# Kernel tuning notes

Hardware: AMD Instinct MI355X
Metric: run time of the kernel (lower is better)

Reference implementation:

```python
import jax, jax.numpy as jnp
import numpy as np

NQ = 4          # n_qubits -> 2**4 = 16 amplitudes
NL = 3          # n_layers
TWO_PI = 2.0 * np.pi
BN_EPS = 1e-5


def _ry_batched(t):
    # t: [B] -> [B,2,2] complex64
    c, s = jnp.cos(t / 2), jnp.sin(t / 2)
    g = jnp.stack([jnp.stack([c, -s], -1), jnp.stack([s, c], -1)], -2)
    return g.astype(jnp.complex64)


def _ry(t):
    c, s = jnp.cos(t / 2), jnp.sin(t / 2)
    return jnp.stack([jnp.stack([c, -s]), jnp.stack([s, c])]).astype(jnp.complex64)


def _rz(t):
    e = jnp.stack([jnp.exp(-0.5j * t), jnp.exp(0.5j * t)]).astype(jnp.complex64)
    return jnp.diag(e)


def _apply_1q(state, gate, wire, batched):
    # state: [B,2,2,2,2]; gate: [2,2] or [B,2,2]
    s = jnp.moveaxis(state, wire + 1, -1)
    if batched:
        s = jnp.einsum('bij,b...j->b...i', gate, s)
    else:
        s = jnp.einsum('ij,...j->...i', gate, s)
    return jnp.moveaxis(s, -1, wire + 1)


def _apply_cnot(state, c, t):
    s = jnp.moveaxis(state, (c + 1, t + 1), (-2, -1))
    s = jnp.stack([s[..., 0, :], s[..., 1, ::-1]], axis=-2)  # flip target when control=1
    return jnp.moveaxis(s, (-2, -1), (c + 1, t + 1))


def _circuit(angles, weights):
    # angles: [B, NQ] float32; weights: [NL, NQ, 2]
    B = angles.shape[0]
    state = jnp.zeros((B,) + (2,) * NQ, jnp.complex64)
    state = state.at[(slice(None),) + (0,) * NQ].set(1.0)
    # input encoding RYs (per-sample angles -> batched gates)
    for i in range(NQ):
        state = _apply_1q(state, _ry_batched(angles[:, i]), i, True)
    for layer in range(NL):
        for i in range(NQ):
            state = _apply_1q(state, _ry(weights[layer, i, 0]), i, False)
            state = _apply_1q(state, _rz(weights[layer, i, 1]), i, False)
        for i in range(NQ - 1):
            state = _apply_cnot(state, i, i + 1)
        state = _apply_cnot(state, NQ - 1, 0)
    probs = jnp.abs(state) ** 2  # [B,2,2,2,2] real
    zs = []
    for i in range(NQ):
        axes = tuple(a for a in range(1, NQ + 1) if a != i + 1)
        pm = probs.sum(axis=axes)  # [B,2]
        zs.append(pm[:, 0] - pm[:, 1])
    return jnp.stack(zs, -1).astype(jnp.float32)  # [B,NQ]


def setup_inputs() -> dict:
    key = jax.random.key(0)
    ks = jax.random.split(key, 4)
    B = 524288
    x = jax.random.normal(ks[0], (B, 16), jnp.float32)
    weights = jax.random.normal(ks[1], (NL, NQ, 2), jnp.float32)
    fc_w = jax.random.normal(ks[2], (4, NQ), jnp.float32) / np.sqrt(NQ)
    fc_b = jax.random.normal(ks[3], (4,), jnp.float32) * 0.01
    gamma = jnp.ones((4,), jnp.float32)
    beta = jnp.zeros((4,), jnp.float32)
    return {"x": x, "weights": weights, "fc_w": fc_w, "fc_b": fc_b,
            "gamma": gamma, "beta": beta}


def reference(x, weights, fc_w, fc_b, gamma, beta):
    inp = x.reshape(x.shape[0], -1)[:, :NQ]
    mn, mx = inp.min(), inp.max()  # global min/max as in the torch code
    angles = TWO_PI * (inp - mn) / (mx - mn + 1e-8)
    q = _circuit(angles, weights)                # [B,4] PauliZ expvals
    out = q @ fc_w.T + fc_b                      # Linear(4,4)
    mean = out.mean(0)
    var = out.var(0)                             # biased, as torch BN training
    return gamma * (out - mean) / jnp.sqrt(var + BN_EPS) + beta
```

## Files before the change

kernel.cpp:

```cpp
#include <hip/hip_runtime.h>
#include <math.h>

#define TWO_PI_F 6.28318530717958647692f
#define BN_EPS_F 1e-5f
#define NB1 2048
#define NB2 1024
#define NT 256

#define BMIN_OFF 256
#define BMAX_OFF 2304
#define TAB_OFF 4352
#define SSLOT_OFF 4992

__global__ __launch_bounds__(NT) void k1_scan_tab(const float* __restrict__ x,
                                                  const float* __restrict__ w,
                                                  const float* __restrict__ fc_w,
                                                  float* __restrict__ wsf, int B) {
  int r = blockIdx.x * NT + threadIdx.x;
  float fmn = __builtin_inff(), fmx = -__builtin_inff();
  if (r < B) {
    float4 v = *(const float4*)(x + (size_t)r * 16);
    fmn = fminf(fminf(v.x, v.y), fminf(v.z, v.w));
    fmx = fmaxf(fmaxf(v.x, v.y), fmaxf(v.z, v.w));
  }
#pragma unroll
  for (int d = 32; d; d >>= 1) {
    fmn = fminf(fmn, __shfl_down(fmn, d));
    fmx = fmaxf(fmx, __shfl_down(fmx, d));
  }
  __shared__ float smn[4], smx[4];
  int wv = threadIdx.x >> 6, ln = threadIdx.x & 63;
  if (ln == 0) { smn[wv] = fmn; smx[wv] = fmx; }
  __syncthreads();
  if (threadIdx.x == 0) {
    wsf[BMIN_OFF + blockIdx.x] =
        fminf(fminf(smn[0], smn[1]), fminf(smn[2], smn[3]));
    wsf[BMAX_OFF + blockIdx.x] =
        fmaxf(fmaxf(smx[0], smx[1]), fmaxf(smx[2], smx[3]));
  }

  if (blockIdx.x == 0) {
    int tid = threadIdx.x;
    if (tid < 16) {
      float sr[16], si[16];
#pragma unroll
      for (int k = 0; k < 16; ++k) { sr[k] = (k == tid) ? 1.f : 0.f; si[k] = 0.f; }
#pragma unroll
      for (int l = 0; l < 3; ++l) {
#pragma unroll
        for (int i = 0; i < 4; ++i) {
          const int m = 8 >> i;
          float ryc, rys, rzc, rzs;
          __sincosf(0.5f * w[(l * 4 + i) * 2 + 0], &rys, &ryc);
          __sincosf(0.5f * w[(l * 4 + i) * 2 + 1], &rzs, &rzc);
#pragma unroll
          for (int k = 0; k < 16; ++k) {
            if (!(k & m)) {
              int k1 = k | m;
              float a0r = sr[k], a0i = si[k], a1r = sr[k1], a1i = si[k1];
              sr[k] = ryc * a0r - rys * a1r;
              si[k] = ryc * a0i - rys * a1i;
              sr[k1] = rys * a0r + ryc * a1r;
              si[k1] = rys * a0i + ryc * a1i;
            }
          }
#pragma unroll
          for (int k = 0; k < 16; ++k) {
            float ps = (k & m) ? rzs : -rzs;
            float rr = sr[k], ii = si[k];
            sr[k] = rr * rzc - ii * ps;
            si[k] = rr * ps + ii * rzc;
          }
        }
#pragma unroll
        for (int c = 0; c < 4; ++c) {
          const int mc = 8 >> c;
          const int mt = 8 >> ((c + 1) & 3);
#pragma unroll
          for (int k = 0; k < 16; ++k) {
            if ((k & mc) && !(k & mt)) {
              int k2 = k | mt;
              float tt;
              tt = sr[k]; sr[k] = sr[k2]; sr[k2] = tt;
              tt = si[k]; si[k] = si[k2]; si[k2] = tt;
            }
          }
        }
      }
#pragma unroll
      for (int k = 0; k < 16; ++k) {
        wsf[TAB_OFF + tid * 16 + k] = sr[k];
        wsf[TAB_OFF + 256 + tid * 16 + k] = si[k];
      }
    } else if (tid == 16) {
      for (int k = 0; k < 16; ++k)
        for (int j = 0; j < 4; ++j) {
          float s = 0.f;
          for (int i = 0; i < 4; ++i)
            s += fc_w[j * 4 + i] * ((k & (8 >> i)) ? -1.f : 1.f);
          wsf[TAB_OFF + 512 + k * 4 + j] = s;
        }
    }
  }
}

__device__ __forceinline__ void qfc_pair(const float* __restrict__ tab,
                                         const float* c0, const float* s0,
                                         const float* c1, const float* s1,
                                         float* o0, float* o1) {
  const float* __restrict__ Ur = tab;
  const float* __restrict__ Ui = tab + 256;
  const float* __restrict__ At = tab + 512;
  float A01_0[4] = {c0[0] * c0[1], c0[0] * s0[1], s0[0] * c0[1], s0[0] * s0[1]};
  float A23_0[4] = {c0[2] * c0[3], c0[2] * s0[3], s0[2] * c0[3], s0[2] * s0[3]};
  float A01_1[4] = {c1[0] * c1[1], c1[0] * s1[1], s1[0] * c1[1], s1[0] * s1[1]};
  float A23_1[4] = {c1[2] * c1[3], c1[2] * s1[3], s1[2] * c1[3], s1[2] * s1[3]};
  float yr0[16], yi0[16], yr1[16], yi1[16];
#pragma unroll
  for (int k = 0; k < 16; ++k) { yr0[k] = yi0[k] = yr1[k] = yi1[k] = 0.f; }
#pragma unroll
  for (int a = 0; a < 16; ++a) {
    float va0 = A01_0[a >> 2] * A23_0[a & 3];
    float va1 = A01_1[a >> 2] * A23_1[a & 3];
#pragma unroll
    for (int k = 0; k < 16; ++k) {
      float ur = Ur[a * 16 + k], ui = Ui[a * 16 + k];
      yr0[k] = fmaf(ur, va0, yr0[k]);
      yi0[k] = fmaf(ui, va0, yi0[k]);
      yr1[k] = fmaf(ur, va1, yr1[k]);
      yi1[k] = fmaf(ui, va1, yi1[k]);
    }
  }
#pragma unroll
  for (int j = 0; j < 4; ++j) { o0[j] = 0.f; o1[j] = 0.f; }
#pragma unroll
  for (int k = 0; k < 16; ++k) {
    float p0 = fmaf(yr0[k], yr0[k], yi0[k] * yi0[k]);
    float p1 = fmaf(yr1[k], yr1[k], yi1[k] * yi1[k]);
#pragma unroll
    for (int j = 0; j < 4; ++j) {
      float av = At[k * 4 + j];
      o0[j] = fmaf(av, p0, o0[j]);
      o1[j] = fmaf(av, p1, o1[j]);
    }
  }
}

__global__ __launch_bounds__(NT) void k2_main(const float* __restrict__ x,
                                              const float* __restrict__ wsf,
                                              float* __restrict__ sslot,
                                              float* __restrict__ out, int B) {
  const int tid = threadIdx.x;
  const int gtid = blockIdx.x * NT + tid;
  const int H = NB2 * NT;
  const int wv = tid >> 6, ln = tid & 63;
  const float* __restrict__ tab = wsf + TAB_OFF;

  float gm = __builtin_inff(), gM = -__builtin_inff();
#pragma unroll
  for (int q = 0; q < NB1 / 64; ++q) {
    int i = ln + q * 64;
    gm = fminf(gm, wsf[BMIN_OFF + i]);
    gM = fmaxf(gM, wsf[BMAX_OFF + i]);
  }
#pragma unroll
  for (int d = 32; d; d >>= 1) {
    gm = fminf(gm, __shfl_down(gm, d));
    gM = fmaxf(gM, __shfl_down(gM, d));
  }
  gm = __shfl(gm, 0);
  gM = __shfl(gM, 0);
  const float ssc = TWO_PI_F * 0.5f / (gM - gm + 1e-8f);

  const int s0 = gtid, s1 = gtid + H;
  const bool h0 = s0 < B, h1 = s1 < B;
  float4 xa = h0 ? *(const float4*)(x + (size_t)s0 * 16) : make_float4(0, 0, 0, 0);
  float4 xb = h1 ? *(const float4*)(x + (size_t)s1 * 16) : make_float4(0, 0, 0, 0);

  float a0[4] = {xa.x, xa.y, xa.z, xa.w};
  float a1[4] = {xb.x, xb.y, xb.z, xb.w};
  float c0[4], sn0[4], c1[4], sn1[4];
#pragma unroll
  for (int i = 0; i < 4; ++i) {
    __sincosf((a0[i] - gm) * ssc, &sn0[i], &c0[i]);
    __sincosf((a1[i] - gm) * ssc, &sn1[i], &c1[i]);
  }
  float o0[4], o1[4];
  qfc_pair(tab, c0, sn0, c1, sn1, o0, o1);

  if (h0)
    *(float4*)(out + (size_t)s0 * 4) = make_float4(o0[0], o0[1], o0[2], o0[3]);
  if (h1)
    *(float4*)(out + (size_t)s1 * 4) = make_float4(o1[0], o1[1], o1[2], o1[3]);

  float vals[8];
#pragma unroll
  for (int j = 0; j < 4; ++j) {
    float v0 = h0 ? o0[j] : 0.f, v1 = h1 ? o1[j] : 0.f;
    vals[j] = v0 + v1;
    vals[4 + j] = fmaf(v0, v0, v1 * v1);
  }
#pragma unroll
  for (int j = 0; j < 8; ++j) {
#pragma unroll
    for (int d = 32; d; d >>= 1) vals[j] += __shfl_down(vals[j], d);
  }
  __shared__ float red[4][8];
  if (ln == 0) {
#pragma unroll
    for (int j = 0; j < 8; ++j) red[wv][j] = vals[j];
  }
  __syncthreads();
  if (tid < 8) {
    sslot[blockIdx.x * 8 + tid] =
        red[0][tid] + red[1][tid] + red[2][tid] + red[3][tid];
  }
}

__global__ __launch_bounds__(NT) void k3_final(float* __restrict__ out,
                                               const float* __restrict__ sslot,
                                               const float* __restrict__ gamma,
                                               const float* __restrict__ beta,
                                               int B) {
  const int tid = threadIdx.x;
  const int gtid = blockIdx.x * NT + tid;
  const int H = NB2 * NT;
  const int ln = tid & 63;

  float v = 0.f;
#pragma unroll
  for (int k = 0; k < (NB2 * 8) / 64; ++k) v += sslot[k * 64 + ln];
#pragma unroll
  for (int d = 32; d >= 8; d >>= 1) v += __shfl_down(v, d);
  float st[8];
#pragma unroll
  for (int j = 0; j < 8; ++j) st[j] = __shfl(v, j);

  const float inv = 1.0f / (float)B;
  float sc[4], sh[4];
#pragma unroll
  for (int j = 0; j < 4; ++j) {
    float mean = st[j] * inv;
    float var = st[4 + j] * inv - mean * mean;
    float is = rsqrtf(var + BN_EPS_F);
    sc[j] = gamma[j] * is;
    sh[j] = beta[j] - mean * sc[j];
  }
#pragma unroll
  for (int p = 0; p < 2; ++p) {
    int s = gtid + p * H;
    if (s < B) {
      float4 q = *(float4*)(out + (size_t)s * 4);
      *(float4*)(out + (size_t)s * 4) =
          make_float4(fmaf(q.x, sc[0], sh[0]), fmaf(q.y, sc[1], sh[1]),
                      fmaf(q.z, sc[2], sh[2]), fmaf(q.w, sc[3], sh[3]));
    }
  }
}

extern "C" void kernel_launch(void* const* d_in, const int* in_sizes, int n_in,
                              void* d_out, int out_size, void* d_ws, size_t ws_size,
                              hipStream_t stream) {
  const float* x = (const float*)d_in[0];
  const float* w = (const float*)d_in[1];
  const float* fc_w = (const float*)d_in[2];
  const float* gamma = (const float*)d_in[4];
  const float* beta = (const float*)d_in[5];
  float* out = (float*)d_out;
  float* wsf = (float*)d_ws;
  int B = in_sizes[0] / 16;

  k1_scan_tab<<<NB1, NT, 0, stream>>>(x, w, fc_w, wsf, B);
  k2_main<<<NB2, NT, 0, stream>>>(x, wsf, wsf + SSLOT_OFF, out, B);
  k3_final<<<NB2, NT, 0, stream>>>(out, wsf + SSLOT_OFF, gamma, beta, B);
}
```

Measured before the change: 113.6 us.

## Precompute quadratic-form coefficients so per-sample output is a 100-term contraction

The output expectation values are quadratic in the real product-state amplitudes, so the unitary and FC weights are folded into 100x4 symmetric coefficients, computed once in block 0 of the first kernel. Each sample then needs only 100 products times 4 FMAs instead of a 16x16 complex matvec plus a probability projection. The main kernel now uses one sample per thread over many more blocks, reads min/max in a single wave and broadcasts it through shared memory, and the final kernel loops over a variable slot count. The trade-off is a serial extra step at the end of the table kernel and many more partial-sum slots for the final reduction to read.

```diff
diff --git a/kernel.cpp b/kernel.cpp
--- a/kernel.cpp
+++ b/kernel.cpp
@@ -4,13 +4,13 @@
 #define TWO_PI_F 6.28318530717958647692f
 #define BN_EPS_F 1e-5f
 #define NB1 2048
-#define NB2 1024
 #define NT 256
 
 #define BMIN_OFF 256
 #define BMAX_OFF 2304
 #define TAB_OFF 4352
-#define SSLOT_OFF 4992
+#define CQ_OFF 4928
+#define SSLOT_OFF 5376
 
 __global__ __launch_bounds__(NT) void k1_scan_tab(const float* __restrict__ x,
                                                   const float* __restrict__ w,
@@ -102,110 +102,119 @@
         }
     }
   }
-}
-
-__device__ __forceinline__ void qfc_pair(const float* __restrict__ tab,
-                                         const float* c0, const float* s0,
-                                         const float* c1, const float* s1,
-                                         float* o0, float* o1) {
-  const float* __restrict__ Ur = tab;
-  const float* __restrict__ Ui = tab + 256;
-  const float* __restrict__ At = tab + 512;
-  float A01_0[4] = {c0[0] * c0[1], c0[0] * s0[1], s0[0] * c0[1], s0[0] * s0[1]};
-  float A23_0[4] = {c0[2] * c0[3], c0[2] * s0[3], s0[2] * c0[3], s0[2] * s0[3]};
-  float A01_1[4] = {c1[0] * c1[1], c1[0] * s1[1], s1[0] * c1[1], s1[0] * s1[1]};
-  float A23_1[4] = {c1[2] * c1[3], c1[2] * s1[3], s1[2] * c1[3], s1[2] * s1[3]};
-  float yr0[16], yi0[16], yr1[16], yi1[16];
-#pragma unroll
-  for (int k = 0; k < 16; ++k) { yr0[k] = yi0[k] = yr1[k] = yi1[k] = 0.f; }
-#pragma unroll
-  for (int a = 0; a < 16; ++a) {
-    float va0 = A01_0[a >> 2] * A23_0[a & 3];
-    float va1 = A01_1[a >> 2] * A23_1[a & 3];
-#pragma unroll
-    for (int k = 0; k < 16; ++k) {
-      float ur = Ur[a * 16 + k], ui = Ui[a * 16 + k];
-      yr0[k] = fmaf(ur, va0, yr0[k]);
-      yi0[k] = fmaf(ui, va0, yi0[k]);
-      yr1[k] = fmaf(ur, va1, yr1[k]);
-      yi1[k] = fmaf(ui, va1, yi1[k]);
-    }
-  }
-#pragma unroll
-  for (int j = 0; j < 4; ++j) { o0[j] = 0.f; o1[j] = 0.f; }
-#pragma unroll
-  for (int k = 0; k < 16; ++k) {
-    float p0 = fmaf(yr0[k], yr0[k], yi0[k] * yi0[k]);
-    float p1 = fmaf(yr1[k], yr1[k], yi1[k] * yi1[k]);
-#pragma unroll
-    for (int j = 0; j < 4; ++j) {
-      float av = At[k * 4 + j];
-      o0[j] = fmaf(av, p0, o0[j]);
-      o1[j] = fmaf(av, p1, o1[j]);
-    }
-  }
-}
-
-__global__ __launch_bounds__(NT) void k2_main(const float* __restrict__ x,
-                                              const float* __restrict__ wsf,
-                                              float* __restrict__ sslot,
-                                              float* __restrict__ out, int B) {
+
+  __syncthreads();
+  if (blockIdx.x == 0 && threadIdx.x < 100) {
+    const int tid = threadIdx.x;
+    const int p = tid / 10, q = tid % 10;
+    int pu, pv, qu, qv;
+    if (p < 4) { pu = 0; pv = p; }
+    else if (p < 7) { pu = 1; pv = p - 3; }
+    else if (p < 9) { pu = 2; pv = p - 5; }
+    else { pu = 3; pv = 3; }
+    if (q < 4) { qu = 0; qv = q; }
+    else if (q < 7) { qu = 1; qv = q - 3; }
+    else if (q < 9) { qu = 2; qv = q - 5; }
+    else { qu = 3; qv = 3; }
+    const float* __restrict__ Tr = wsf + TAB_OFF;
+    const float* __restrict__ Ti = wsf + TAB_OFF + 256;
+    const float* __restrict__ At = wsf + TAB_OFF + 512;
+    const int nh = (pu == pv) ? 1 : 2;
+    const int nl = (qu == qv) ? 1 : 2;
+    float c[4] = {0.f, 0.f, 0.f, 0.f};
+    for (int hh = 0; hh < nh; ++hh) {
+      int ha = hh ? pv : pu, hb = hh ? pu : pv;
+      for (int ll = 0; ll < nl; ++ll) {
+        int la = ll ? qv : qu, lb = ll ? qu : qv;
+        int a = 4 * ha + la, b = 4 * hb + lb;
+        for (int k = 0; k < 16; ++k) {
+          float rr = Tr[a * 16 + k] * Tr[b * 16 + k] +
+                     Ti[a * 16 + k] * Ti[b * 16 + k];
+#pragma unroll
+          for (int j = 0; j < 4; ++j) c[j] = fmaf(At[k * 4 + j], rr, c[j]);
+        }
+      }
+    }
+#pragma unroll
+    for (int j = 0; j < 4; ++j) wsf[CQ_OFF + tid * 4 + j] = c[j];
+  }
+}
+
+__global__ __launch_bounds__(NT, 8) void k2_main(const float* __restrict__ x,
+                                                 const float* __restrict__ wsf,
+                                                 float* __restrict__ sslot,
+                                                 float* __restrict__ out, int B) {
   const int tid = threadIdx.x;
-  const int gtid = blockIdx.x * NT + tid;
-  const int H = NB2 * NT;
+  const int s0 = blockIdx.x * NT + tid;
   const int wv = tid >> 6, ln = tid & 63;
-  const float* __restrict__ tab = wsf + TAB_OFF;
-
-  float gm = __builtin_inff(), gM = -__builtin_inff();
-#pragma unroll
-  for (int q = 0; q < NB1 / 64; ++q) {
-    int i = ln + q * 64;
-    gm = fminf(gm, wsf[BMIN_OFF + i]);
-    gM = fmaxf(gM, wsf[BMAX_OFF + i]);
-  }
-#pragma unroll
-  for (int d = 32; d; d >>= 1) {
-    gm = fminf(gm, __shfl_down(gm, d));
-    gM = fmaxf(gM, __shfl_down(gM, d));
-  }
-  gm = __shfl(gm, 0);
-  gM = __shfl(gM, 0);
-  const float ssc = TWO_PI_F * 0.5f / (gM - gm + 1e-8f);
-
-  const int s0 = gtid, s1 = gtid + H;
-  const bool h0 = s0 < B, h1 = s1 < B;
+  const float* __restrict__ Cq = wsf + CQ_OFF;
+  __shared__ float sbc[2];
+  __shared__ float red[4][8];
+
+  const bool h0 = s0 < B;
   float4 xa = h0 ? *(const float4*)(x + (size_t)s0 * 16) : make_float4(0, 0, 0, 0);
-  float4 xb = h1 ? *(const float4*)(x + (size_t)s1 * 16) : make_float4(0, 0, 0, 0);
-
-  float a0[4] = {xa.x, xa.y, xa.z, xa.w};
-  float a1[4] = {xb.x, xb.y, xb.z, xb.w};
-  float c0[4], sn0[4], c1[4], sn1[4];
-#pragma unroll
-  for (int i = 0; i < 4; ++i) {
-    __sincosf((a0[i] - gm) * ssc, &sn0[i], &c0[i]);
-    __sincosf((a1[i] - gm) * ssc, &sn1[i], &c1[i]);
-  }
-  float o0[4], o1[4];
-  qfc_pair(tab, c0, sn0, c1, sn1, o0, o1);
+
+  if (wv == 0) {
+    float gm = __builtin_inff(), gM = -__builtin_inff();
+#pragma unroll
+    for (int q = 0; q < NB1 / 64; ++q) {
+      gm = fminf(gm, wsf[BMIN_OFF + ln + q * 64]);
+      gM = fmaxf(gM, wsf[BMAX_OFF + ln + q * 64]);
+    }
+#pragma unroll
+    for (int d = 32; d; d >>= 1) {
+      gm = fminf(gm, __shfl_down(gm, d));
+      gM = fmaxf(gM, __shfl_down(gM, d));
+    }
+    if (ln == 0) { sbc[0] = gm; sbc[1] = gM; }
+  }
+  __syncthreads();
+  const float gm = sbc[0];
+  const float ssc = TWO_PI_F * 0.5f / (sbc[1] - gm + 1e-8f);
+
+  float cc[4], sn[4];
+  {
+    float a[4] = {xa.x, xa.y, xa.z, xa.w};
+#pragma unroll
+    for (int i = 0; i < 4; ++i) __sincosf((a[i] - gm) * ssc, &sn[i], &cc[i]);
+  }
+  float A01[4] = {cc[0] * cc[1], cc[0] * sn[1], sn[0] * cc[1], sn[0] * sn[1]};
+  float A23[4] = {cc[2] * cc[3], cc[2] * sn[3], sn[2] * cc[3], sn[2] * sn[3]};
+  float P01[10], P23[10];
+  P01[0] = A01[0] * A01[0]; P01[1] = A01[0] * A01[1]; P01[2] = A01[0] * A01[2];
+  P01[3] = A01[0] * A01[3]; P01[4] = A01[1] * A01[1]; P01[5] = A01[1] * A01[2];
+  P01[6] = A01[1] * A01[3]; P01[7] = A01[2] * A01[2]; P01[8] = A01[2] * A01[3];
+  P01[9] = A01[3] * A01[3];
+  P23[0] = A23[0] * A23[0]; P23[1] = A23[0] * A23[1]; P23[2] = A23[0] * A23[2];
+  P23[3] = A23[0] * A23[3]; P23[4] = A23[1] * A23[1]; P23[5] = A23[1] * A23[2];
+  P23[6] = A23[1] * A23[3]; P23[7] = A23[2] * A23[2]; P23[8] = A23[2] * A23[3];
+  P23[9] = A23[3] * A23[3];
+
+  float o[4] = {0.f, 0.f, 0.f, 0.f};
+#pragma unroll
+  for (int t = 0; t < 100; ++t) {
+    float vv = P01[t / 10] * P23[t % 10];
+    o[0] = fmaf(Cq[t * 4 + 0], vv, o[0]);
+    o[1] = fmaf(Cq[t * 4 + 1], vv, o[1]);
+    o[2] = fmaf(Cq[t * 4 + 2], vv, o[2]);
+    o[3] = fmaf(Cq[t * 4 + 3], vv, o[3]);
+  }
 
   if (h0)
-    *(float4*)(out + (size_t)s0 * 4) = make_float4(o0[0], o0[1], o0[2], o0[3]);
-  if (h1)
-    *(float4*)(out + (size_t)s1 * 4) = make_float4(o1[0], o1[1], o1[2], o1[3]);
+    *(float4*)(out + (size_t)s0 * 4) = make_float4(o[0], o[1], o[2], o[3]);
 
   float vals[8];
 #pragma unroll
   for (int j = 0; j < 4; ++j) {
-    float v0 = h0 ? o0[j] : 0.f, v1 = h1 ? o1[j] : 0.f;
-    vals[j] = v0 + v1;
-    vals[4 + j] = fmaf(v0, v0, v1 * v1);
+    float v = h0 ? o[j] : 0.f;
+    vals[j] = v;
+    vals[4 + j] = v * v;
   }
 #pragma unroll
   for (int j = 0; j < 8; ++j) {
 #pragma unroll
     for (int d = 32; d; d >>= 1) vals[j] += __shfl_down(vals[j], d);
   }
-  __shared__ float red[4][8];
   if (ln == 0) {
 #pragma unroll
     for (int j = 0; j < 8; ++j) red[wv][j] = vals[j];
@@ -221,27 +230,28 @@
                                                const float* __restrict__ sslot,
                                                const float* __restrict__ gamma,
                                                const float* __restrict__ beta,
-                                               int B) {
+                                               int B, int nb2) {
   const int tid = threadIdx.x;
   const int gtid = blockIdx.x * NT + tid;
-  const int H = NB2 * NT;
-  const int ln = tid & 63;
-
-  float v = 0.f;
-#pragma unroll
-  for (int k = 0; k < (NB2 * 8) / 64; ++k) v += sslot[k * 64 + ln];
-#pragma unroll
-  for (int d = 32; d >= 8; d >>= 1) v += __shfl_down(v, d);
-  float st[8];
-#pragma unroll
-  for (int j = 0; j < 8; ++j) st[j] = __shfl(v, j);
+  const int H = gridDim.x * NT;
+  const int wv = tid >> 6, ln = tid & 63;
+  __shared__ float sst[8];
+
+  if (wv == 0) {
+    float v = 0.f;
+    for (int e = ln; e < nb2 * 8; e += 64) v += sslot[e];
+#pragma unroll
+    for (int d = 32; d >= 8; d >>= 1) v += __shfl_down(v, d);
+    if (ln < 8) sst[ln] = v;
+  }
+  __syncthreads();
 
   const float inv = 1.0f / (float)B;
   float sc[4], sh[4];
 #pragma unroll
   for (int j = 0; j < 4; ++j) {
-    float mean = st[j] * inv;
-    float var = st[4 + j] * inv - mean * mean;
+    float mean = sst[j] * inv;
+    float var = sst[4 + j] * inv - mean * mean;
     float is = rsqrtf(var + BN_EPS_F);
     sc[j] = gamma[j] * is;
     sh[j] = beta[j] - mean * sc[j];
@@ -270,7 +280,10 @@
   float* wsf = (float*)d_ws;
   int B = in_sizes[0] / 16;
 
+  int nb2 = (B + NT - 1) / NT;
+  int nb3 = (B + 2 * NT - 1) / (2 * NT);
+
   k1_scan_tab<<<NB1, NT, 0, stream>>>(x, w, fc_w, wsf, B);
-  k2_main<<<NB2, NT, 0, stream>>>(x, wsf, wsf + SSLOT_OFF, out, B);
-  k3_final<<<NB2, NT, 0, stream>>>(out, wsf + SSLOT_OFF, gamma, beta, B);
-}
+  k2_main<<<nb2, NT, 0, stream>>>(x, wsf, wsf + SSLOT_OFF, out, B);
+  k3_final<<<nb3, NT, 0, stream>>>(out, wsf + SSLOT_OFF, gamma, beta, B, nb2);
+}
```

Result: slower. 171.9 us (+51.3%).
